# Kernel optimization log

Hardware: AMD Instinct MI355X
Metric: run time of the kernel (lower is better)

Reference implementation:

```python
import jax, jax.numpy as jnp
import numpy as np

D = 2048      # hidden_size
W = 4         # kernel_size
DG = 2048     # generator hidden size (no reduction)

def setup_inputs() -> dict:
    key = jax.random.key(0)
    k1, k2, k3, k4 = jax.random.split(key, 4)
    x = jax.random.normal(k1, (2, 4096, D), dtype=jnp.float32)
    # Linear weights stored torch-style [out, in]; scaled small for sane activations
    w1 = jax.random.normal(k2, (DG, D), dtype=jnp.float32) * 0.02
    w2 = jax.random.normal(k3, (D * W, DG), dtype=jnp.float32) * 0.02
    b2 = jax.random.normal(k4, (D * W,), dtype=jnp.float32) * 0.02
    return {"x": x, "w1": w1, "w2": w2, "b2": b2}

def reference(x, w1, w2, b2):
    B, T, Dh = x.shape
    # kernel generator: w2(silu(w1 @ x)) + b2 -> per-position kernels [B,T,D,W]
    h = jax.nn.silu(jnp.einsum('btd,gd->btg', x, w1))
    flat = jnp.einsum('btg,kg->btk', h, w2) + b2
    kernels = flat.reshape(B, T, Dh, W)
    # causal depthwise dynamic conv: y[b,t,d] = sum_w x[b, t-(W-1)+w, d] * k[b,t,d,w]
    xp = jnp.pad(x, ((0, 0), (W - 1, 0), (0, 0)))
    y = xp[:, 0:T, :] * kernels[..., 0]
    for w in range(1, W):  # small fixed-width loop over kernel taps
        y = y + xp[:, w:w + T, :] * kernels[..., w]
    return jax.nn.silu(y)
```

## Files before the change

kernel.cpp:

```cpp
#include <hip/hip_runtime.h>
#include <hip/hip_bf16.h>
#include <cstdint>

#define D_DIM  2048
#define T_DIM  4096
#define B_DIM  2
#define M_DIM  8192
#define DG_DIM 2048
#define N2_DIM 8192
#define K_DIM  2048

typedef __bf16 bf16x8 __attribute__((ext_vector_type(8)));
typedef __bf16 bf16x4 __attribute__((ext_vector_type(4)));
typedef float  f32x4  __attribute__((ext_vector_type(4)));

__device__ __forceinline__ void gload_lds16(const void* g, void* l) {
  __builtin_amdgcn_global_load_lds(
      (__attribute__((address_space(1))) void*)g,
      (__attribute__((address_space(3))) void*)l, 16, 0, 0);
}

__device__ __forceinline__ float silu_f(float a) {
  return a / (1.f + __expf(-a));
}

__global__ void cast_f32_bf16(const float* __restrict__ src,
                              __bf16* __restrict__ dst, int n4) {
  int i = blockIdx.x * blockDim.x + threadIdx.x;
  if (i >= n4) return;
  float4 v = ((const float4*)src)[i];
  bf16x4 o;
  o[0] = (__bf16)v.x; o[1] = (__bf16)v.y; o[2] = (__bf16)v.z; o[3] = (__bf16)v.w;
  ((bf16x4*)dst)[i] = o;
}

__global__ void cast_permute_w2(const float* __restrict__ src,
                                __bf16* __restrict__ dst, int n4) {
  int i = blockIdx.x * blockDim.x + threadIdx.x;
  if (i >= n4) return;
  const int row = i >> 9;
  const int pos = i & 511;
  const int blk = row >> 7, within = row & 127;
  const int wn = (within >> 6) & 1, j = (within >> 4) & 3, ln = within & 15;
  const int d = blk * 32 + wn * 16 + ln;
  const int k = 4 * d + j;
  float4 v = ((const float4*)src)[(size_t)k * 512 + pos];
  bf16x4 o;
  o[0] = (__bf16)v.x; o[1] = (__bf16)v.y; o[2] = (__bf16)v.z; o[3] = (__bf16)v.w;
  ((bf16x4*)dst)[i] = o;
}


__global__ __launch_bounds__(256) void gemm1_silu(
    const __bf16* __restrict__ A, const __bf16* __restrict__ B,
    __bf16* __restrict__ H) {
  constexpr int K = K_DIM, N = DG_DIM;
  __shared__ __bf16 sA[128 * 64];
  __shared__ __bf16 sB[128 * 64];
  const int tid  = threadIdx.x;
  const int lane = tid & 63;
  const int wv   = tid >> 6;
  const int wm   = wv >> 1, wn = wv & 1;
  const int ln   = lane & 15, qd = lane >> 4;
  const int m0 = blockIdx.y * 128, n0 = blockIdx.x * 128;

  f32x4 acc[4][4] = {};

  const int g  = lane >> 3;
  const int cl = lane & 7;
  const int cg = cl ^ g;
  const __bf16* gA[4];
  const __bf16* gB[4];
  int loff[4];
#pragma unroll
  for (int inst = 0; inst < 4; inst++) {
    const int r = (inst * 4 + wv) * 8 + g;
    gA[inst]   = A + (size_t)(m0 + r) * K + cg * 8;
    gB[inst]   = B + (size_t)(n0 + r) * K + cg * 8;
    loff[inst] = ((inst * 4 + wv) * 64 + lane) * 8;
  }

  for (int k0 = 0; k0 < K; k0 += 64) {
#pragma unroll
    for (int inst = 0; inst < 4; inst++)
      gload_lds16(gA[inst] + k0, sA + loff[inst]);
#pragma unroll
    for (int inst = 0; inst < 4; inst++)
      gload_lds16(gB[inst] + k0, sB + loff[inst]);
    __syncthreads();
#pragma unroll
    for (int h = 0; h < 2; h++) {
      bf16x8 af[4], bfr[4];
#pragma unroll
      for (int i = 0; i < 4; i++) {
        const int row = wm * 64 + i * 16 + ln;
        af[i] = *(const bf16x8*)(sA + row * 64 + (((h << 2) + qd) ^ (row & 7)) * 8);
      }
#pragma unroll
      for (int j = 0; j < 4; j++) {
        const int row = wn * 64 + j * 16 + ln;
        bfr[j] = *(const bf16x8*)(sB + row * 64 + (((h << 2) + qd) ^ (row & 7)) * 8);
      }
#pragma unroll
      for (int i = 0; i < 4; i++)
#pragma unroll
        for (int j = 0; j < 4; j++)
          acc[i][j] = __builtin_amdgcn_mfma_f32_16x16x32_bf16(af[i], bfr[j],
                                                              acc[i][j], 0, 0, 0);
    }
    __syncthreads();
  }

#pragma unroll
  for (int i = 0; i < 4; i++) {
#pragma unroll
    for (int j = 0; j < 4; j++) {
      const int col = n0 + wn * 64 + j * 16 + ln;
#pragma unroll
      for (int r = 0; r < 4; r++) {
        const int row = m0 + wm * 64 + i * 16 + qd * 4 + r;
        H[(size_t)row * N + col] = (__bf16)silu_f(acc[i][j][r]);
      }
    }
  }
}

__global__ __launch_bounds__(256) void gemm2_conv_silu(
    const __bf16* __restrict__ A, const __bf16* __restrict__ B,
    const float* __restrict__ b2, const float* __restrict__ x,
    float* __restrict__ out) {
  constexpr int K = K_DIM;
  __shared__ __bf16 sA[128 * 64];
  __shared__ __bf16 sB[128 * 64];
  const int tid  = threadIdx.x;
  const int lane = tid & 63;
  const int wv   = tid >> 6;
  const int wm   = wv >> 1, wn = wv & 1;
  const int ln   = lane & 15, qd = lane >> 4;
  const int m0 = blockIdx.y * 128, n0 = blockIdx.x * 128;

  f32x4 acc[4][4] = {};

  const int g  = lane >> 3;
  const int cl = lane & 7;
  const int cg = cl ^ g;
  const __bf16* gA[4];
  const __bf16* gB[4];
  int loff[4];
#pragma unroll
  for (int inst = 0; inst < 4; inst++) {
    const int r = (inst * 4 + wv) * 8 + g;
    gA[inst]   = A + (size_t)(m0 + r) * K + cg * 8;
    gB[inst]   = B + (size_t)(n0 + r) * K + cg * 8;
    loff[inst] = ((inst * 4 + wv) * 64 + lane) * 8;
  }

  for (int k0 = 0; k0 < K; k0 += 64) {
#pragma unroll
    for (int inst = 0; inst < 4; inst++)
      gload_lds16(gA[inst] + k0, sA + loff[inst]);
#pragma unroll
    for (int inst = 0; inst < 4; inst++)
      gload_lds16(gB[inst] + k0, sB + loff[inst]);
    __syncthreads();
#pragma unroll
    for (int h = 0; h < 2; h++) {
      bf16x8 af[4], bfr[4];
#pragma unroll
      for (int i = 0; i < 4; i++) {
        const int row = wm * 64 + i * 16 + ln;
        af[i] = *(const bf16x8*)(sA + row * 64 + (((h << 2) + qd) ^ (row & 7)) * 8);
      }
#pragma unroll
      for (int j = 0; j < 4; j++) {
        const int row = wn * 64 + j * 16 + ln;
        bfr[j] = *(const bf16x8*)(sB + row * 64 + (((h << 2) + qd) ^ (row & 7)) * 8);
      }
#pragma unroll
      for (int i = 0; i < 4; i++)
#pragma unroll
        for (int j = 0; j < 4; j++)
          acc[i][j] = __builtin_amdgcn_mfma_f32_16x16x32_bf16(af[i], bfr[j],
                                                              acc[i][j], 0, 0, 0);
    }
    __syncthreads();
  }

  const int d = (n0 >> 2) + wn * 16 + ln;
  const float4 bias = *(const float4*)(b2 + 4 * d);

#pragma unroll
  for (int i = 0; i < 4; i++) {
    const int m_base = m0 + wm * 64 + i * 16 + qd * 4;
    const int b  = m_base >> 12;
    const int tb = m_base & 4095;
    float xv[7];
#pragma unroll
    for (int s = 0; s < 7; s++) {
      const int tp = tb + s - 3;
      xv[s] = (tp >= 0) ? x[((size_t)((b << 12) + tp)) * D_DIM + d] : 0.f;
    }
#pragma unroll
    for (int r = 0; r < 4; r++) {
      float y = (acc[i][0][r] + bias.x) * xv[r + 0]
              + (acc[i][1][r] + bias.y) * xv[r + 1]
              + (acc[i][2][r] + bias.z) * xv[r + 2]
              + (acc[i][3][r] + bias.w) * xv[r + 3];
      out[(size_t)(m_base + r) * D_DIM + d] = silu_f(y);
    }
  }
}

extern "C" void kernel_launch(void* const* d_in, const int* in_sizes, int n_in,
                              void* d_out, int out_size, void* d_ws, size_t ws_size,
                              hipStream_t stream) {
  (void)in_sizes; (void)n_in; (void)out_size; (void)ws_size;
  const float* x  = (const float*)d_in[0];
  const float* w1 = (const float*)d_in[1];
  const float* w2 = (const float*)d_in[2];
  const float* b2 = (const float*)d_in[3];
  float* out = (float*)d_out;

  __bf16* xb  = (__bf16*)d_ws;
  __bf16* w1b = xb  + (size_t)M_DIM * D_DIM;
  __bf16* w2b = w1b + (size_t)DG_DIM * D_DIM;
  __bf16* hb  = w2b + (size_t)N2_DIM * DG_DIM;

  {
    int n4 = M_DIM * D_DIM / 4;
    cast_f32_bf16<<<(n4 + 255) / 256, 256, 0, stream>>>(x, xb, n4);
  }
  {
    int n4 = DG_DIM * D_DIM / 4;
    cast_f32_bf16<<<(n4 + 255) / 256, 256, 0, stream>>>(w1, w1b, n4);
  }
  {
    int n4 = N2_DIM * DG_DIM / 4;
    cast_permute_w2<<<(n4 + 255) / 256, 256, 0, stream>>>(w2, w2b, n4);
  }

  gemm1_silu<<<dim3(DG_DIM / 128, M_DIM / 128), 256, 0, stream>>>(xb, w1b, hb);
  gemm2_conv_silu<<<dim3(N2_DIM / 128, M_DIM / 128), 256, 0, stream>>>(
      hb, w2b, b2, x, out);
}
```

Before: 538.5 us.

## Use 256x256 tiles with 8 waves and a double-buffered ping-pong GEMM pipeline

Both GEMMs move from 128x128 tiles with 4 waves and a single LDS buffer to 256x256 tiles with 8 waves. Global-to-LDS loads are split into half-tiles and prefetched two stages ahead. Each k-step is broken into four MFMA phases separated by explicit barriers and priority bumps, so loads overlap with compute. The w2 permutation is changed to match the new 64-column-per-block layout that the fused conv epilogue expects. The cost is 128KB of LDS per block and much higher register pressure from 32 accumulators, which may limit occupancy to one block per CU.

```diff
diff --git a/kernel.cpp b/kernel.cpp
--- a/kernel.cpp
+++ b/kernel.cpp
@@ -1,5 +1,4 @@
 #include <hip/hip_runtime.h>
-#include <hip/hip_bf16.h>
 #include <cstdint>
 
 #define D_DIM  2048
@@ -9,6 +8,7 @@
 #define DG_DIM 2048
 #define N2_DIM 8192
 #define K_DIM  2048
+#define NT_TILES (K_DIM / 64)
 
 typedef __bf16 bf16x8 __attribute__((ext_vector_type(8)));
 typedef __bf16 bf16x4 __attribute__((ext_vector_type(4)));
@@ -40,10 +40,13 @@
   if (i >= n4) return;
   const int row = i >> 9;
   const int pos = i & 511;
-  const int blk = row >> 7, within = row & 127;
-  const int wn = (within >> 6) & 1, j = (within >> 4) & 3, ln = within & 15;
-  const int d = blk * 32 + wn * 16 + ln;
-  const int k = 4 * d + j;
+  const int blk = row >> 8;
+  const int cw  = row & 255;
+  const int j   = cw >> 6;
+  const int wn  = (cw >> 4) & 3;
+  const int ln  = cw & 15;
+  const int d   = blk * 64 + wn * 16 + ln;
+  const int k   = 4 * d + j;
   float4 v = ((const float4*)src)[(size_t)k * 512 + pos];
   bf16x4 o;
   o[0] = (__bf16)v.x; o[1] = (__bf16)v.y; o[2] = (__bf16)v.z; o[3] = (__bf16)v.w;
@@ -51,147 +54,194 @@
 }
 
 
-__global__ __launch_bounds__(256) void gemm1_silu(
+__device__ __forceinline__ void stage_unit(const __bf16* src0, const __bf16* src1,
+                                           __bf16* sX, int s, int hf,
+                                           int lq0, int lq1) {
+  const int k0 = (s < NT_TILES) ? (s * 64) : 0;
+  __bf16* dst = sX + ((s & 1) * 2 + hf) * 8192;
+  const size_t goff = (size_t)hf * 128 * K_DIM + k0;
+  gload_lds16(src0 + goff, dst + lq0);
+  gload_lds16(src1 + goff, dst + lq1);
+}
+
+__device__ __forceinline__ void read4(bf16x8 dst[4][2], const __bf16* base,
+                                      const int off[4][2]) {
+#pragma unroll
+  for (int i = 0; i < 4; i++) {
+    dst[i][0] = *(const bf16x8*)(base + off[i][0]);
+    dst[i][1] = *(const bf16x8*)(base + off[i][1]);
+  }
+}
+
+__device__ __forceinline__ void read2(bf16x8 dst[2][2], const __bf16* base,
+                                      const int off[2][2]) {
+#pragma unroll
+  for (int j = 0; j < 2; j++) {
+    dst[j][0] = *(const bf16x8*)(base + off[j][0]);
+    dst[j][1] = *(const bf16x8*)(base + off[j][1]);
+  }
+}
+
+__device__ __forceinline__ void mmaq(f32x4 acc[8][4], int ib, int jb,
+                                     const bf16x8 a[4][2], const bf16x8 b[2][2]) {
+#pragma unroll
+  for (int kk = 0; kk < 2; kk++)
+#pragma unroll
+    for (int i = 0; i < 4; i++)
+#pragma unroll
+      for (int j = 0; j < 2; j++)
+        acc[ib + i][jb + j] = __builtin_amdgcn_mfma_f32_16x16x32_bf16(
+            a[i][kk], b[j][kk], acc[ib + i][jb + j], 0, 0, 0);
+}
+
+__device__ __forceinline__ void phase_mid() {
+  __builtin_amdgcn_s_barrier();
+  asm volatile("s_waitcnt lgkmcnt(0)" ::: "memory");
+  __builtin_amdgcn_sched_barrier(0);
+  __builtin_amdgcn_s_setprio(1);
+}
+
+__device__ __forceinline__ void phase_end() {
+  __builtin_amdgcn_s_setprio(0);
+  __builtin_amdgcn_s_barrier();
+}
+
+__device__ __forceinline__ void gemm_core(const __bf16* __restrict__ A,
+                                          const __bf16* __restrict__ B,
+                                          int m0, int n0,
+                                          __bf16* sA, __bf16* sB,
+                                          f32x4 acc[8][4]) {
+  constexpr int K = K_DIM;
+  const int t    = threadIdx.x;
+  const int lane = t & 63;
+  const int wv   = t >> 6;
+  const int wm   = wv >> 2;
+  const int wn   = wv & 3;
+  const int ln   = lane & 15, qd = lane >> 4;
+
+  const __bf16 *a_src0, *a_src1, *b_src0, *b_src1;
+  int lq0, lq1;
+  {
+    int q = t, row = q >> 3, cg = (q & 7) ^ (row & 7);
+    a_src0 = A + (size_t)(m0 + row) * K + cg * 8;
+    b_src0 = B + (size_t)(n0 + row) * K + cg * 8;
+    lq0 = q * 8;
+    q = 512 + t; row = q >> 3; cg = (q & 7) ^ (row & 7);
+    a_src1 = A + (size_t)(m0 + row) * K + cg * 8;
+    b_src1 = B + (size_t)(n0 + row) * K + cg * 8;
+    lq1 = q * 8;
+  }
+
+  int aoff[4][2], boff[2][2];
+#pragma unroll
+  for (int i = 0; i < 4; i++)
+#pragma unroll
+    for (int kk = 0; kk < 2; kk++) {
+      const int row = wm * 16 + i * 32 + ln;
+      aoff[i][kk] = row * 64 + (((kk * 4 + qd) ^ (row & 7)) << 3);
+    }
+#pragma unroll
+  for (int j = 0; j < 2; j++)
+#pragma unroll
+    for (int kk = 0; kk < 2; kk++) {
+      const int row = j * 64 + wn * 16 + ln;
+      boff[j][kk] = row * 64 + (((kk * 4 + qd) ^ (row & 7)) << 3);
+    }
+
+  bf16x8 aL[4][2], aH[4][2], b0[2][2], b1[2][2];
+
+  stage_unit(a_src0, a_src1, sA, 0, 0, lq0, lq1);
+  stage_unit(b_src0, b_src1, sB, 0, 0, lq0, lq1);
+  stage_unit(a_src0, a_src1, sA, 0, 1, lq0, lq1);
+  stage_unit(b_src0, b_src1, sB, 0, 1, lq0, lq1);
+  stage_unit(a_src0, a_src1, sA, 1, 0, lq0, lq1);
+  stage_unit(b_src0, b_src1, sB, 1, 0, lq0, lq1);
+  stage_unit(a_src0, a_src1, sA, 1, 1, lq0, lq1);
+  asm volatile("s_waitcnt vmcnt(6)" ::: "memory");
+  __builtin_amdgcn_s_barrier();
+
+  for (int t0 = 0; t0 < NT_TILES; ++t0) {
+    const int p = t0 & 1;
+    const __bf16* A0h = sA + p * 16384;
+    const __bf16* B0h = sB + p * 16384;
+
+    read4(aL, A0h, aoff);
+    read2(b0, B0h, boff);
+    stage_unit(b_src0, b_src1, sB, t0 + 1, 1, lq0, lq1);
+    phase_mid();
+    mmaq(acc, 0, 0, aL, b0);
+    phase_end();
+
+    read4(aH, A0h + 8192, aoff);
+    stage_unit(a_src0, a_src1, sA, t0 + 2, 0, lq0, lq1);
+    phase_mid();
+    mmaq(acc, 4, 0, aH, b0);
+    phase_end();
+
+    read2(b1, B0h + 8192, boff);
+    stage_unit(b_src0, b_src1, sB, t0 + 2, 0, lq0, lq1);
+    phase_mid();
+    mmaq(acc, 0, 2, aL, b1);
+    phase_end();
+
+    stage_unit(a_src0, a_src1, sA, t0 + 2, 1, lq0, lq1);
+    asm volatile("s_waitcnt vmcnt(6)" ::: "memory");
+    __builtin_amdgcn_s_barrier();
+    __builtin_amdgcn_s_setprio(1);
+    mmaq(acc, 4, 2, aH, b1);
+    __builtin_amdgcn_s_setprio(0);
+    __builtin_amdgcn_s_barrier();
+  }
+  asm volatile("s_waitcnt vmcnt(0)" ::: "memory");
+}
+
+__global__ __launch_bounds__(512) void gemm1_silu(
     const __bf16* __restrict__ A, const __bf16* __restrict__ B,
     __bf16* __restrict__ H) {
-  constexpr int K = K_DIM, N = DG_DIM;
-  __shared__ __bf16 sA[128 * 64];
-  __shared__ __bf16 sB[128 * 64];
-  const int tid  = threadIdx.x;
-  const int lane = tid & 63;
-  const int wv   = tid >> 6;
-  const int wm   = wv >> 1, wn = wv & 1;
+  __shared__ __bf16 sA[4 * 8192];
+  __shared__ __bf16 sB[4 * 8192];
+  const int m0 = blockIdx.y * 256, n0 = blockIdx.x * 256;
+  f32x4 acc[8][4] = {};
+  gemm_core(A, B, m0, n0, sA, sB, acc);
+
+  const int lane = threadIdx.x & 63;
+  const int wv   = threadIdx.x >> 6;
+  const int wm   = wv >> 2, wn = wv & 3;
   const int ln   = lane & 15, qd = lane >> 4;
-  const int m0 = blockIdx.y * 128, n0 = blockIdx.x * 128;
-
-  f32x4 acc[4][4] = {};
-
-  const int g  = lane >> 3;
-  const int cl = lane & 7;
-  const int cg = cl ^ g;
-  const __bf16* gA[4];
-  const __bf16* gB[4];
-  int loff[4];
-#pragma unroll
-  for (int inst = 0; inst < 4; inst++) {
-    const int r = (inst * 4 + wv) * 8 + g;
-    gA[inst]   = A + (size_t)(m0 + r) * K + cg * 8;
-    gB[inst]   = B + (size_t)(n0 + r) * K + cg * 8;
-    loff[inst] = ((inst * 4 + wv) * 64 + lane) * 8;
-  }
-
-  for (int k0 = 0; k0 < K; k0 += 64) {
-#pragma unroll
-    for (int inst = 0; inst < 4; inst++)
-      gload_lds16(gA[inst] + k0, sA + loff[inst]);
-#pragma unroll
-    for (int inst = 0; inst < 4; inst++)
-      gload_lds16(gB[inst] + k0, sB + loff[inst]);
-    __syncthreads();
-#pragma unroll
-    for (int h = 0; h < 2; h++) {
-      bf16x8 af[4], bfr[4];
-#pragma unroll
-      for (int i = 0; i < 4; i++) {
-        const int row = wm * 64 + i * 16 + ln;
-        af[i] = *(const bf16x8*)(sA + row * 64 + (((h << 2) + qd) ^ (row & 7)) * 8);
-      }
-#pragma unroll
-      for (int j = 0; j < 4; j++) {
-        const int row = wn * 64 + j * 16 + ln;
-        bfr[j] = *(const bf16x8*)(sB + row * 64 + (((h << 2) + qd) ^ (row & 7)) * 8);
-      }
-#pragma unroll
-      for (int i = 0; i < 4; i++)
-#pragma unroll
-        for (int j = 0; j < 4; j++)
-          acc[i][j] = __builtin_amdgcn_mfma_f32_16x16x32_bf16(af[i], bfr[j],
-                                                              acc[i][j], 0, 0, 0);
-    }
-    __syncthreads();
-  }
-
-#pragma unroll
-  for (int i = 0; i < 4; i++) {
+#pragma unroll
+  for (int i = 0; i < 8; i++) {
+    const int row0 = m0 + wm * 16 + i * 32 + qd * 4;
 #pragma unroll
     for (int j = 0; j < 4; j++) {
-      const int col = n0 + wn * 64 + j * 16 + ln;
-#pragma unroll
-      for (int r = 0; r < 4; r++) {
-        const int row = m0 + wm * 64 + i * 16 + qd * 4 + r;
-        H[(size_t)row * N + col] = (__bf16)silu_f(acc[i][j][r]);
-      }
-    }
-  }
-}
-
-__global__ __launch_bounds__(256) void gemm2_conv_silu(
+      const int col = n0 + wn * 16 + j * 64 + ln;
+#pragma unroll
+      for (int r = 0; r < 4; r++)
+        H[(size_t)(row0 + r) * DG_DIM + col] = (__bf16)silu_f(acc[i][j][r]);
+    }
+  }
+}
+
+__global__ __launch_bounds__(512) void gemm2_conv_silu(
     const __bf16* __restrict__ A, const __bf16* __restrict__ B,
     const float* __restrict__ b2, const float* __restrict__ x,
     float* __restrict__ out) {
-  constexpr int K = K_DIM;
-  __shared__ __bf16 sA[128 * 64];
-  __shared__ __bf16 sB[128 * 64];
-  const int tid  = threadIdx.x;
-  const int lane = tid & 63;
-  const int wv   = tid >> 6;
-  const int wm   = wv >> 1, wn = wv & 1;
+  __shared__ __bf16 sA[4 * 8192];
+  __shared__ __bf16 sB[4 * 8192];
+  const int m0 = blockIdx.y * 256, n0 = blockIdx.x * 256;
+  f32x4 acc[8][4] = {};
+  gemm_core(A, B, m0, n0, sA, sB, acc);
+
+  const int lane = threadIdx.x & 63;
+  const int wv   = threadIdx.x >> 6;
+  const int wm   = wv >> 2, wn = wv & 3;
   const int ln   = lane & 15, qd = lane >> 4;
-  const int m0 = blockIdx.y * 128, n0 = blockIdx.x * 128;
-
-  f32x4 acc[4][4] = {};
-
-  const int g  = lane >> 3;
-  const int cl = lane & 7;
-  const int cg = cl ^ g;
-  const __bf16* gA[4];
-  const __bf16* gB[4];
-  int loff[4];
-#pragma unroll
-  for (int inst = 0; inst < 4; inst++) {
-    const int r = (inst * 4 + wv) * 8 + g;
-    gA[inst]   = A + (size_t)(m0 + r) * K + cg * 8;
-    gB[inst]   = B + (size_t)(n0 + r) * K + cg * 8;
-    loff[inst] = ((inst * 4 + wv) * 64 + lane) * 8;
-  }
-
-  for (int k0 = 0; k0 < K; k0 += 64) {
-#pragma unroll
-    for (int inst = 0; inst < 4; inst++)
-      gload_lds16(gA[inst] + k0, sA + loff[inst]);
-#pragma unroll
-    for (int inst = 0; inst < 4; inst++)
-      gload_lds16(gB[inst] + k0, sB + loff[inst]);
-    __syncthreads();
-#pragma unroll
-    for (int h = 0; h < 2; h++) {
-      bf16x8 af[4], bfr[4];
-#pragma unroll
-      for (int i = 0; i < 4; i++) {
-        const int row = wm * 64 + i * 16 + ln;
-        af[i] = *(const bf16x8*)(sA + row * 64 + (((h << 2) + qd) ^ (row & 7)) * 8);
-      }
-#pragma unroll
-      for (int j = 0; j < 4; j++) {
-        const int row = wn * 64 + j * 16 + ln;
-        bfr[j] = *(const bf16x8*)(sB + row * 64 + (((h << 2) + qd) ^ (row & 7)) * 8);
-      }
-#pragma unroll
-      for (int i = 0; i < 4; i++)
-#pragma unroll
-        for (int j = 0; j < 4; j++)
-          acc[i][j] = __builtin_amdgcn_mfma_f32_16x16x32_bf16(af[i], bfr[j],
-                                                              acc[i][j], 0, 0, 0);
-    }
-    __syncthreads();
-  }
 
   const int d = (n0 >> 2) + wn * 16 + ln;
   const float4 bias = *(const float4*)(b2 + 4 * d);
 
 #pragma unroll
-  for (int i = 0; i < 4; i++) {
-    const int m_base = m0 + wm * 64 + i * 16 + qd * 4;
+  for (int i = 0; i < 8; i++) {
+    const int m_base = m0 + wm * 16 + i * 32 + qd * 4;
     const int b  = m_base >> 12;
     const int tb = m_base & 4095;
     float xv[7];
@@ -239,7 +289,7 @@
     cast_permute_w2<<<(n4 + 255) / 256, 256, 0, stream>>>(w2, w2b, n4);
   }
 
-  gemm1_silu<<<dim3(DG_DIM / 128, M_DIM / 128), 256, 0, stream>>>(xb, w1b, hb);
-  gemm2_conv_silu<<<dim3(N2_DIM / 128, M_DIM / 128), 256, 0, stream>>>(
+  gemm1_silu<<<dim3(DG_DIM / 256, M_DIM / 256), 512, 0, stream>>>(xb, w1b, hb);
+  gemm2_conv_silu<<<dim3(N2_DIM / 256, M_DIM / 256), 512, 0, stream>>>(
       hb, w2b, b2, x, out);
 }
```

Result: faster. 498.3 us (-7.5%).
